# Kernel optimization log

Measured on AMD Instinct MI355X. Metric: run time of the kernel, lower is better.

Reference implementation:

```python
import jax, jax.numpy as jnp
import numpy as np

B, N, C, K = 8, 49104, 90, 1000  # batch, anchors, classes, pre-NMS top-k cap
NEG = -1e9


def _decode(reg, anc):
    # anchors ltrb -> cxcywh, apply reg, back to ltrb (matches decode_boxes)
    l, t, r, b = anc[..., 0], anc[..., 1], anc[..., 2], anc[..., 3]
    w_a, h_a = r - l, b - t
    cx_a, cy_a = l + w_a / 2, t + h_a / 2
    cx = cx_a + reg[..., 0] * w_a
    cy = cy_a + reg[..., 1] * h_a
    w = w_a * jnp.exp(reg[..., 2])
    h = h_a * jnp.exp(reg[..., 3])
    left, top = cx - w / 2, cy - h / 2
    return jnp.stack([left, top, left + w, top + h], -1)


def _iou(boxes):  # [K,4] -> [K,K]
    area = (boxes[:, 2] - boxes[:, 0]) * (boxes[:, 3] - boxes[:, 1])
    lt = jnp.maximum(boxes[:, None, :2], boxes[None, :, :2])
    rb = jnp.minimum(boxes[:, None, 2:], boxes[None, :, 2:])
    wh = jnp.clip(rb - lt, 0.0)
    inter = wh[..., 0] * wh[..., 1]
    return inter / (area[:, None] + area[None, :] - inter + 1e-9)


def _per_image(cls, reg, anchors, size, size_ori, score_thresh, nms_thresh):
    scores = jnp.max(cls, axis=-1)                       # [N]
    labels = jnp.argmax(cls, axis=-1).astype(jnp.int32)  # [N]
    valid = scores >= score_thresh
    boxes = _decode(reg, anchors)                        # [N,4] ltrb
    H = size[0].astype(jnp.float32)
    W = size[1].astype(jnp.float32)
    x = jnp.clip(boxes[..., 0::2], 0.0, W - 1.0)
    y = jnp.clip(boxes[..., 1::2], 0.0, H - 1.0)
    boxes = jnp.stack([x[..., 0], y[..., 0], x[..., 1], y[..., 1]], -1)
    # fixed-size substitute for nonzero(): take top-K by masked score
    ms = jnp.where(valid, scores, NEG)
    top_s, idx = jax.lax.top_k(ms, K)
    b, l, v = boxes[idx], labels[idx], valid[idx]        # [K,4],[K],[K]
    # batched_nms trick: offset boxes per class so classes never overlap
    off = l.astype(jnp.float32) * (jnp.maximum(W, H) + 1.0)
    iou = _iou(b + off[:, None])                         # [K,K]
    ar = jnp.arange(K)
    def body(i, supp):
        keep_i = v[i] & jnp.logical_not(supp[i])
        return supp | (keep_i & (iou[i] > nms_thresh) & (ar > i))
    supp = jax.lax.fori_loop(0, K, body, jnp.zeros((K,), bool))
    keep = v & jnp.logical_not(supp)
    scale = size_ori[0].astype(jnp.float32) / H
    b = b * scale
    out5 = jnp.concatenate(
        [jnp.where(keep[:, None], b, 0.0), jnp.where(keep, top_s, 0.0)[:, None]], -1)
    return out5, jnp.where(keep, l, -1), keep


def setup_inputs() -> dict:
    key = jax.random.key(0)
    k1, k2, k3, k4, k5, k6 = jax.random.split(key, 6)
    classifications = jax.random.uniform(k1, (B, N, C), dtype=jnp.float32)
    regressions = jax.random.normal(k2, (B, N, 4), dtype=jnp.float32) * 0.1
    cx = jax.random.uniform(k3, (N,), minval=0.0, maxval=512.0)
    cy = jax.random.uniform(k4, (N,), minval=0.0, maxval=512.0)
    w = jax.random.uniform(k5, (N,), minval=16.0, maxval=256.0)
    h = jax.random.uniform(k6, (N,), minval=16.0, maxval=256.0)
    anchors = jnp.stack([cx - w / 2, cy - h / 2, cx + w / 2, cy + h / 2], -1)
    return {
        'classifications': classifications,
        'regressions': regressions,
        'anchors': anchors,
        'image_sizes': jnp.full((B, 2), 512, dtype=jnp.int32),
        'image_sizes_ori': jnp.full((B, 2), 768, dtype=jnp.int32),
        'score_thresh': jnp.float32(0.999),
        'nms_thresh': jnp.float32(0.5),
    }


def reference(classifications, regressions, anchors, image_sizes, image_sizes_ori, score_thresh, nms_thresh):
    out5, labels, keep = jax.vmap(
        _per_image, in_axes=(0, 0, None, 0, 0, None, None))(
        classifications, regressions, anchors, image_sizes, image_sizes_ori,
        score_thresh, nms_thresh)
    return out5, labels, keep
```

## Files before the change

kernel.cpp:

```cpp
#include <hip/hip_runtime.h>
#include <stdint.h>

#define NB 8
#define NN 49104
#define NNP 49152
#define NC 90
#define NK 1000
#define KW 16
#define CAP2 8192
#define SEG 1024
#define CHUNK 6144
#define NB2 4352
#define NB2P 5120

typedef unsigned long long u64;

__global__ void k_score(const float* __restrict__ cls,
                        const float* __restrict__ thr_p,
                        u64* __restrict__ keys) {
  __shared__ float lds[64 * NC];
  int b = blockIdx.y;
  int t0 = blockIdx.x * 64;
  int acnt = NN - t0; if (acnt > 64) acnt = 64;
  const float4* src = (const float4*)(cls + ((size_t)b * NN + t0) * NC);
  float4* dst = (float4*)lds;
  int elems4 = acnt * NC / 4;
  for (int t = threadIdx.x; t < elems4; t += 256) dst[t] = src[t];
  __syncthreads();
  int a = threadIdx.x >> 2, q = threadIdx.x & 3;
  float best = -1e30f; int bc = 0;
  if (a < acnt) {
    for (int c = q; c < NC; c += 4) {
      float v = lds[a * NC + c];
      if (v > best) { best = v; bc = c; }
    }
    float ov; int oc;
    ov = __shfl_xor(best, 1); oc = __shfl_xor(bc, 1);
    if (ov > best || (ov == best && oc < bc)) { best = ov; bc = oc; }
    ov = __shfl_xor(best, 2); oc = __shfl_xor(bc, 2);
    if (ov > best || (ov == best && oc < bc)) { best = ov; bc = oc; }
  }
  if (q == 0) {
    unsigned idx = (unsigned)(t0 + a);
    u64 key = 0ULL;
    if (a < acnt && best >= *thr_p)
      key = ((u64)__float_as_uint(best) << 32) |
            ((u64)(0xFFFFu - idx) << 16) | (u64)(unsigned)bc;
    keys[(size_t)b * NNP + idx] = key;
  }
}

__global__ __launch_bounds__(1024) void k_compact(const u64* __restrict__ keys,
                                                  u64* __restrict__ ckeys) {
  __shared__ unsigned scnt;
  int tid = threadIdx.x;
  int lane = tid & 63;
  int b = blockIdx.y, chunk = blockIdx.x;
  if (tid == 0) scnt = 0u;
  __syncthreads();
  const u64* src = keys + (size_t)b * NNP + (size_t)chunk * CHUNK;
  u64* dst = ckeys + (size_t)b * CAP2 + (size_t)chunk * SEG;
  u64 k0 = src[tid], k1 = src[tid + 1024], k2 = src[tid + 2048];
  u64 k3 = src[tid + 3072], k4 = src[tid + 4096], k5 = src[tid + 5120];
  u64 lmask = (1ULL << lane) - 1ULL;
  u64 kk[6] = {k0, k1, k2, k3, k4, k5};
#pragma unroll
  for (int j = 0; j < 6; j++) {
    u64 key = kk[j];
    bool valid = key != 0ULL;
    u64 m = __ballot(valid);
    if (m) {
      int leader = (int)__ffsll((unsigned long long)m) - 1;
      unsigned base = 0;
      if (lane == leader) base = atomicAdd(&scnt, (unsigned)__popcll(m));
      base = __shfl(base, leader);
      if (valid) {
        unsigned pos = base + (unsigned)__popcll(m & lmask);
        if (pos < SEG) dst[pos] = key;
      }
    }
  }
  __syncthreads();
  unsigned total = scnt; if (total > SEG) total = SEG;
  for (unsigned t = total + tid; t < SEG; t += 1024) dst[t] = 0ULL;
}

__device__ __forceinline__ void decode_box(const float4 rg, const float4 an,
                                           float W, float H, float* out) {
#pragma clang fp contract(off)
  float l = an.x, t = an.y, r = an.z, bo = an.w;
  float wa = r - l, ha = bo - t;
  float cxa = l + wa * 0.5f, cya = t + ha * 0.5f;
  float cx = cxa + rg.x * wa;
  float cy = cya + rg.y * ha;
  float w = wa * expf(rg.z);
  float h = ha * expf(rg.w);
  float left = cx - w * 0.5f, top = cy - h * 0.5f;
  float right = left + w, botm = top + h;
  out[0] = fminf(fmaxf(left, 0.f), W - 1.f);
  out[1] = fminf(fmaxf(top, 0.f), H - 1.f);
  out[2] = fminf(fmaxf(right, 0.f), W - 1.f);
  out[3] = fminf(fmaxf(botm, 0.f), H - 1.f);
}

__global__ __launch_bounds__(1024) void k_sortsel(
    const u64* __restrict__ ckeys,
    const float* __restrict__ regs, const float* __restrict__ anch,
    const int* __restrict__ isz, const int* __restrict__ iszo,
    int* __restrict__ nvalid, float4* __restrict__ topoff,
    int* __restrict__ toplabel, float* __restrict__ out) {
  __shared__ u64 cand[CAP2];
  __shared__ u64 outk[CAP2];
  __shared__ unsigned hist[NB2P];
  __shared__ unsigned wsum[16];
  __shared__ unsigned scnt;
  int tid = threadIdx.x;
  int lane = tid & 63, wid = tid >> 6;
  int b = blockIdx.x;
  for (int i = tid; i < NB2P; i += 1024) hist[i] = 0u;
  if (tid == 0) scnt = 0u;
  __syncthreads();
  const ulonglong4* kv = (const ulonglong4*)(ckeys + (size_t)b * CAP2);
  ulonglong4 c0 = kv[tid], c1 = kv[tid + 1024];
  u64 lmask = (1ULL << lane) - 1ULL;
  u64 kk[8] = {c0.x, c0.y, c0.z, c0.w, c1.x, c1.y, c1.z, c1.w};
#pragma unroll
  for (int j = 0; j < 8; j++) {
    u64 key = kk[j];
    bool valid = key != 0ULL;
    u64 m = __ballot(valid);
    if (m) {
      int leader = (int)__ffsll((unsigned long long)m) - 1;
      unsigned base = 0;
      if (lane == leader) base = atomicAdd(&scnt, (unsigned)__popcll(m));
      base = __shfl(base, leader);
      if (valid) {
        unsigned pos = base + (unsigned)__popcll(m & lmask);
        if (pos < CAP2) cand[pos] = key;
        unsigned bin = (0x3F800000u - (unsigned)(key >> 32) - 1u) >> 2;
        if (bin >= NB2) bin = NB2 - 1;
        atomicAdd(&hist[bin], 1u);
      }
    }
  }
  __syncthreads();

  int base5 = tid * 5;
  unsigned mysum = 0;
#pragma unroll
  for (int i = 0; i < 5; i++) mysum += hist[base5 + i];
  unsigned v = mysum;
  for (int d = 1; d < 64; d <<= 1) {
    unsigned o = __shfl_up(v, d);
    if (lane >= d) v += o;
  }
  if (lane == 63) wsum[wid] = v;
  __syncthreads();
  if (tid == 0) {
    unsigned acc = 0;
    for (int w2 = 0; w2 < 16; w2++) { unsigned c = wsum[w2]; wsum[w2] = acc; acc += c; }
  }
  __syncthreads();
  unsigned running = wsum[wid] + v - mysum;
#pragma unroll
  for (int i = 0; i < 5; i++) {
    unsigned c = hist[base5 + i];
    hist[base5 + i] = running;
    running += c;
  }
  __syncthreads();

  unsigned total = scnt; if (total > CAP2) total = CAP2;
  for (unsigned p = tid; p < total; p += 1024) {
    u64 key = cand[p];
    unsigned bin = (0x3F800000u - (unsigned)(key >> 32) - 1u) >> 2;
    if (bin >= NB2) bin = NB2 - 1;
    unsigned pos = atomicAdd(&hist[bin], 1u);
    if (pos < CAP2) outk[pos] = key;
  }
  __syncthreads();

  for (int bin = tid; bin < NB2; bin += 1024) {
    unsigned hi = hist[bin];
    unsigned lo = bin ? hist[bin - 1] : 0u;
    if (hi > CAP2) hi = CAP2;
    if (lo > CAP2) lo = CAP2;
    if (hi > lo + 1) {
      for (unsigned i2 = lo + 1; i2 < hi; i2++) {
        u64 kx = outk[i2];
        int j = (int)i2 - 1;
        while (j >= (int)lo && outk[j] < kx) { outk[j + 1] = outk[j]; j--; }
        outk[j + 1] = kx;
      }
    }
  }
  __syncthreads();

  int n = (int)scnt; if (n > NK) n = NK;
  if (tid == 0) nvalid[b] = n;
  float H = (float)isz[b * 2 + 0];
  float W = (float)isz[b * 2 + 1];
  float scale = (float)iszo[b * 2 + 0] / H;
  float offmul = fmaxf(W, H) + 1.0f;
  for (int k = tid; k < n; k += 1024) {
    u64 key = outk[k];
    float sc = __uint_as_float((unsigned)(key >> 32));
    unsigned idx = 0xFFFFu - (unsigned)((key >> 16) & 0xFFFFull);
    int lab = (int)(key & 0xFFFFull);
    float raw[4];
    float4 rg = ((const float4*)regs)[(size_t)b * NN + idx];
    float4 an = ((const float4*)anch)[idx];
    decode_box(rg, an, W, H, raw);
    float off = (float)lab * offmul;
    topoff[(size_t)b * NK + k] =
        make_float4(raw[0] + off, raw[1] + off, raw[2] + off, raw[3] + off);
    toplabel[(size_t)b * NK + k] = lab;
    int g = b * NK + k;
    float* o5 = out + (size_t)g * 5;
    o5[0] = raw[0] * scale; o5[1] = raw[1] * scale;
    o5[2] = raw[2] * scale; o5[3] = raw[3] * scale;
    o5[4] = sc;
    out[(size_t)NB * NK * 5 + g] = (float)lab;
  }
}

__global__ __launch_bounds__(1024) void k_masknms(
    const float4* __restrict__ topoff, const int* __restrict__ toplabel,
    const int* __restrict__ nvalid, const float* __restrict__ thr_p,
    float* __restrict__ out) {
#pragma clang fp contract(off)
  __shared__ float4 bo[NK];
  __shared__ __align__(16) u64 sm[NK * KW];
  __shared__ unsigned short sidx[NK];
  __shared__ unsigned short send[NK];
  __shared__ int lcnt[NC + 1];
  __shared__ int lofs[NC + 1];
  __shared__ int lcur[NC];
  __shared__ u64 nzv[16];
  __shared__ u64 skeep[KW];
  int b = blockIdx.x;
  int tid = threadIdx.x;
  int n = nvalid[b];

  for (int t = tid; t < NK * KW; t += 1024) sm[t] = 0ULL;
  if (tid < 16) nzv[tid] = 0ULL;
  if (tid <= NC) lcnt[tid] = 0;
  for (int t = tid; t < NK; t += 1024) bo[t] = topoff[(size_t)b * NK + t];
  __syncthreads();

  for (int k = tid; k < n; k += 1024)
    atomicAdd(&lcnt[toplabel[(size_t)b * NK + k]], 1);
  __syncthreads();
  if (tid == 0) {
    int acc = 0;
    for (int c = 0; c < NC; c++) { lofs[c] = acc; acc += lcnt[c]; }
    lofs[NC] = acc;
  }
  __syncthreads();
  if (tid < NC) lcur[tid] = lofs[tid];
  __syncthreads();
  for (int k = tid; k < n; k += 1024) {
    int lab = toplabel[(size_t)b * NK + k];
    int pos = atomicAdd(&lcur[lab], 1);
    sidx[pos] = (unsigned short)k;
    send[pos] = (unsigned short)lofs[lab + 1];
  }
  __syncthreads();

  float thr = *thr_p;
  for (int p = tid; p < n; p += 1024) {
    int e = (int)send[p];
    int a = (int)sidx[p];
    for (int q = p + 1; q < e; q++) {
      int c2 = (int)sidx[q];
      int i = a < c2 ? a : c2;
      int j = a < c2 ? c2 : a;
      float4 B = bo[i];
      float4 C = bo[j];
      float x0 = B.x, y0 = B.y, x1 = B.z, y1 = B.w;
      float ai = (x1 - x0) * (y1 - y0);
      float aj = (C.z - C.x) * (C.w - C.y);
      float ltx = fmaxf(x0, C.x), lty = fmaxf(y0, C.y);
      float rbx = fminf(x1, C.z), rby = fminf(y1, C.w);
      float ww = fmaxf(rbx - ltx, 0.f), hh = fmaxf(rby - lty, 0.f);
      float inter = ww * hh;
      float den = ((ai + aj) - inter) + 1e-9f;
      float iou = inter / den;
      if (iou > thr) {
        atomicOr(&sm[(size_t)i * KW + (j >> 6)], 1ULL << (j & 63));
        atomicOr(&nzv[i >> 6], 1ULL << (i & 63));
      }
    }
  }
  __syncthreads();

  if (tid < 16) {
    int base = tid * 64;
    u64 validw;
    if (n <= base) validw = 0ULL;
    else if (n >= base + 64) validw = ~0ULL;
    else validw = (~0ULL) >> (64 - (n - base));
    nzv[tid] &= validw;
  }
  __syncthreads();

  int lane = tid & 63, ml = tid & 15;
  if (tid < 64) {
    int bb2 = ml * 64;
    u64 rem;
    if (n <= bb2) rem = ~0ULL;
    else if (n >= bb2 + 64) rem = 0ULL;
    else rem = (~0ULL) << (n - bb2);
    for (int w = 0; w < 16; w++) {
      unsigned rl = (unsigned)__builtin_amdgcn_readlane((int)(unsigned)rem, w);
      unsigned rh = (unsigned)__builtin_amdgcn_readlane((int)(unsigned)(rem >> 32), w);
      u64 rw = ((u64)rh << 32) | (u64)rl;
      u64 active = nzv[w] & ~rw;
      while (active) {
        int i = (int)__ffsll((unsigned long long)active) - 1;
        active &= active - 1ULL;
        u64 crow = sm[(size_t)(w * 64 + i) * KW + ml];
        rem |= crow;
        unsigned cl = (unsigned)__builtin_amdgcn_readlane((int)(unsigned)crow, w);
        unsigned ch = (unsigned)__builtin_amdgcn_readlane((int)(unsigned)(crow >> 32), w);
        rw |= ((u64)ch << 32) | (u64)cl;
        active &= ~rw;
      }
      if (lane == 0) skeep[w] = ~rw;
    }
  }
  __syncthreads();

  for (int k = tid; k < NK; k += 1024) {
    int g = b * NK + k;
    int keep = (int)((skeep[k >> 6] >> (k & 63)) & 1ULL);
    if (keep) {
      out[(size_t)NB * NK * 6 + g] = 1.0f;
    } else {
      float* o5 = out + (size_t)g * 5;
      o5[0] = 0.f; o5[1] = 0.f; o5[2] = 0.f; o5[3] = 0.f; o5[4] = 0.f;
      out[(size_t)NB * NK * 5 + g] = -1.0f;
      out[(size_t)NB * NK * 6 + g] = 0.0f;
    }
  }
}

extern "C" void kernel_launch(void* const* d_in, const int* in_sizes, int n_in,
                              void* d_out, int out_size, void* d_ws, size_t ws_size,
                              hipStream_t stream) {
  const float* cls = (const float*)d_in[0];
  const float* regs = (const float*)d_in[1];
  const float* anch = (const float*)d_in[2];
  const int* isz = (const int*)d_in[3];
  const int* iszo = (const int*)d_in[4];
  const float* sthr = (const float*)d_in[5];
  const float* nthr = (const float*)d_in[6];
  float* out = (float*)d_out;

  char* p = (char*)d_ws;
  auto alloc = [&](size_t bytes) {
    char* r = p;
    p += (bytes + 255) & ~(size_t)255;
    return r;
  };
  u64* keys = (u64*)alloc((size_t)NB * NNP * 8);
  u64* ckeys = (u64*)alloc((size_t)NB * CAP2 * 8);
  float4* topoff = (float4*)alloc((size_t)NB * NK * 16);
  int* toplabel = (int*)alloc((size_t)NB * NK * 4);
  int* nvalid = (int*)alloc((size_t)NB * 4);

  hipLaunchKernelGGL(k_score, dim3(NNP / 64, NB), dim3(256), 0, stream,
                     cls, sthr, keys);
  hipLaunchKernelGGL(k_compact, dim3(8, NB), dim3(1024), 0, stream,
                     keys, ckeys);
  hipLaunchKernelGGL(k_sortsel, dim3(NB), dim3(1024), 0, stream,
                     ckeys, regs, anch, isz, iszo, nvalid, topoff, toplabel, out);
  hipLaunchKernelGGL(k_masknms, dim3(NB), dim3(1024), 0, stream,
                     topoff, toplabel, nvalid, nthr, out);
}
```

Measured before the change: 59.64 us.

## Fuse compaction into scoring and merge sort-select with NMS kernel

```diff
diff --git a/kernel.cpp b/kernel.cpp
--- a/kernel.cpp
+++ b/kernel.cpp
@@ -9,7 +9,7 @@
 #define KW 16
 #define CAP2 8192
 #define SEG 1024
-#define CHUNK 6144
+#define BPC 96
 #define NB2 4352
 #define NB2P 5120
 
@@ -17,7 +17,8 @@
 
 __global__ void k_score(const float* __restrict__ cls,
                         const float* __restrict__ thr_p,
-                        u64* __restrict__ keys) {
+                        u64* __restrict__ ckeys,
+                        unsigned* __restrict__ segcnt) {
   __shared__ float lds[64 * NC];
   int b = blockIdx.y;
   int t0 = blockIdx.x * 64;
@@ -40,49 +41,28 @@
     ov = __shfl_xor(best, 2); oc = __shfl_xor(bc, 2);
     if (ov > best || (ov == best && oc < bc)) { best = ov; bc = oc; }
   }
-  if (q == 0) {
+  int lane = threadIdx.x & 63;
+  bool valid = (q == 0) && (a < acnt) && (best >= *thr_p);
+  u64 key = 0ULL;
+  if (valid) {
     unsigned idx = (unsigned)(t0 + a);
-    u64 key = 0ULL;
-    if (a < acnt && best >= *thr_p)
-      key = ((u64)__float_as_uint(best) << 32) |
-            ((u64)(0xFFFFu - idx) << 16) | (u64)(unsigned)bc;
-    keys[(size_t)b * NNP + idx] = key;
-  }
-}
-
-__global__ __launch_bounds__(1024) void k_compact(const u64* __restrict__ keys,
-                                                  u64* __restrict__ ckeys) {
-  __shared__ unsigned scnt;
-  int tid = threadIdx.x;
-  int lane = tid & 63;
-  int b = blockIdx.y, chunk = blockIdx.x;
-  if (tid == 0) scnt = 0u;
-  __syncthreads();
-  const u64* src = keys + (size_t)b * NNP + (size_t)chunk * CHUNK;
-  u64* dst = ckeys + (size_t)b * CAP2 + (size_t)chunk * SEG;
-  u64 k0 = src[tid], k1 = src[tid + 1024], k2 = src[tid + 2048];
-  u64 k3 = src[tid + 3072], k4 = src[tid + 4096], k5 = src[tid + 5120];
-  u64 lmask = (1ULL << lane) - 1ULL;
-  u64 kk[6] = {k0, k1, k2, k3, k4, k5};
-#pragma unroll
-  for (int j = 0; j < 6; j++) {
-    u64 key = kk[j];
-    bool valid = key != 0ULL;
-    u64 m = __ballot(valid);
-    if (m) {
-      int leader = (int)__ffsll((unsigned long long)m) - 1;
-      unsigned base = 0;
-      if (lane == leader) base = atomicAdd(&scnt, (unsigned)__popcll(m));
-      base = __shfl(base, leader);
-      if (valid) {
-        unsigned pos = base + (unsigned)__popcll(m & lmask);
-        if (pos < SEG) dst[pos] = key;
-      }
-    }
-  }
-  __syncthreads();
-  unsigned total = scnt; if (total > SEG) total = SEG;
-  for (unsigned t = total + tid; t < SEG; t += 1024) dst[t] = 0ULL;
+    key = ((u64)__float_as_uint(best) << 32) |
+          ((u64)(0xFFFFu - idx) << 16) | (u64)(unsigned)bc;
+  }
+  u64 m = __ballot(valid);
+  if (m) {
+    int leader = (int)__ffsll((unsigned long long)m) - 1;
+    int chunk = blockIdx.x / BPC;
+    unsigned base = 0;
+    if (lane == leader)
+      base = atomicAdd(&segcnt[b * 8 + chunk], (unsigned)__popcll(m));
+    base = __shfl(base, leader);
+    if (valid) {
+      unsigned pos = base + (unsigned)__popcll(m & ((1ULL << lane) - 1ULL));
+      if (pos < SEG)
+        ckeys[(size_t)b * CAP2 + (size_t)chunk * SEG + pos] = key;
+    }
+  }
 }
 
 __device__ __forceinline__ void decode_box(const float4 rg, const float4 an,
@@ -103,45 +83,52 @@
   out[3] = fminf(fmaxf(botm, 0.f), H - 1.f);
 }
 
-__global__ __launch_bounds__(1024) void k_sortsel(
-    const u64* __restrict__ ckeys,
+__global__ __launch_bounds__(1024) void k_sortnms(
+    const u64* __restrict__ ckeys, const unsigned* __restrict__ segcnt,
     const float* __restrict__ regs, const float* __restrict__ anch,
     const int* __restrict__ isz, const int* __restrict__ iszo,
-    int* __restrict__ nvalid, float4* __restrict__ topoff,
-    int* __restrict__ toplabel, float* __restrict__ out) {
-  __shared__ u64 cand[CAP2];
-  __shared__ u64 outk[CAP2];
-  __shared__ unsigned hist[NB2P];
+    const float* __restrict__ nthr_p, float* __restrict__ out) {
+#pragma clang fp contract(off)
+  __shared__ __align__(16) char S[151552];
   __shared__ unsigned wsum[16];
-  __shared__ unsigned scnt;
+  __shared__ unsigned sofs[9];
+  __shared__ int lcnt[NC + 1];
+  __shared__ int lofs[NC + 1];
+  __shared__ int lcur[NC];
+  __shared__ u64 nzv[16];
+  __shared__ u64 skeep[KW];
+
+  u64* cand = (u64*)S;
+  u64* outk = (u64*)(S + 65536);
+  unsigned* hist = (unsigned*)(S + 131072);
+
   int tid = threadIdx.x;
   int lane = tid & 63, wid = tid >> 6;
   int b = blockIdx.x;
+
   for (int i = tid; i < NB2P; i += 1024) hist[i] = 0u;
-  if (tid == 0) scnt = 0u;
-  __syncthreads();
-  const ulonglong4* kv = (const ulonglong4*)(ckeys + (size_t)b * CAP2);
-  ulonglong4 c0 = kv[tid], c1 = kv[tid + 1024];
-  u64 lmask = (1ULL << lane) - 1ULL;
-  u64 kk[8] = {c0.x, c0.y, c0.z, c0.w, c1.x, c1.y, c1.z, c1.w};
-#pragma unroll
-  for (int j = 0; j < 8; j++) {
-    u64 key = kk[j];
-    bool valid = key != 0ULL;
-    u64 m = __ballot(valid);
-    if (m) {
-      int leader = (int)__ffsll((unsigned long long)m) - 1;
-      unsigned base = 0;
-      if (lane == leader) base = atomicAdd(&scnt, (unsigned)__popcll(m));
-      base = __shfl(base, leader);
-      if (valid) {
-        unsigned pos = base + (unsigned)__popcll(m & lmask);
-        if (pos < CAP2) cand[pos] = key;
-        unsigned bin = (0x3F800000u - (unsigned)(key >> 32) - 1u) >> 2;
-        if (bin >= NB2) bin = NB2 - 1;
-        atomicAdd(&hist[bin], 1u);
-      }
-    }
+  if (tid == 0) {
+    unsigned acc = 0;
+    for (int s = 0; s < 8; s++) {
+      unsigned c = segcnt[b * 8 + s]; if (c > SEG) c = SEG;
+      sofs[s] = acc; acc += c;
+    }
+    sofs[8] = acc;
+  }
+  __syncthreads();
+  unsigned total = sofs[8];
+
+  for (int s = 0; s < 8; s++) {
+    unsigned o = sofs[s], c = sofs[s + 1] - o;
+    const u64* srcp = ckeys + (size_t)b * CAP2 + (size_t)s * SEG;
+    for (unsigned i = tid; i < c; i += 1024) cand[o + i] = srcp[i];
+  }
+  __syncthreads();
+
+  for (unsigned p = tid; p < total; p += 1024) {
+    unsigned bin = (0x3F800000u - (unsigned)(cand[p] >> 32) - 1u) >> 2;
+    if (bin >= NB2) bin = NB2 - 1;
+    atomicAdd(&hist[bin], 1u);
   }
   __syncthreads();
 
@@ -170,7 +157,6 @@
   }
   __syncthreads();
 
-  unsigned total = scnt; if (total > CAP2) total = CAP2;
   for (unsigned p = tid; p < total; p += 1024) {
     u64 key = cand[p];
     unsigned bin = (0x3F800000u - (unsigned)(key >> 32) - 1u) >> 2;
@@ -196,8 +182,13 @@
   }
   __syncthreads();
 
-  int n = (int)scnt; if (n > NK) n = NK;
-  if (tid == 0) nvalid[b] = n;
+  int n = (int)total; if (n > NK) n = NK;
+  float4* bo = (float4*)S;
+  unsigned short* llab = (unsigned short*)(S + 16000);
+  unsigned short* sidx = (unsigned short*)(S + 18000);
+  unsigned short* send = (unsigned short*)(S + 20000);
+  u64* sm = (u64*)(S + 22016);
+
   float H = (float)isz[b * 2 + 0];
   float W = (float)isz[b * 2 + 1];
   float scale = (float)iszo[b * 2 + 0] / H;
@@ -212,9 +203,8 @@
     float4 an = ((const float4*)anch)[idx];
     decode_box(rg, an, W, H, raw);
     float off = (float)lab * offmul;
-    topoff[(size_t)b * NK + k] =
-        make_float4(raw[0] + off, raw[1] + off, raw[2] + off, raw[3] + off);
-    toplabel[(size_t)b * NK + k] = lab;
+    bo[k] = make_float4(raw[0] + off, raw[1] + off, raw[2] + off, raw[3] + off);
+    llab[k] = (unsigned short)lab;
     int g = b * NK + k;
     float* o5 = out + (size_t)g * 5;
     o5[0] = raw[0] * scale; o5[1] = raw[1] * scale;
@@ -222,34 +212,14 @@
     o5[4] = sc;
     out[(size_t)NB * NK * 5 + g] = (float)lab;
   }
-}
-
-__global__ __launch_bounds__(1024) void k_masknms(
-    const float4* __restrict__ topoff, const int* __restrict__ toplabel,
-    const int* __restrict__ nvalid, const float* __restrict__ thr_p,
-    float* __restrict__ out) {
-#pragma clang fp contract(off)
-  __shared__ float4 bo[NK];
-  __shared__ __align__(16) u64 sm[NK * KW];
-  __shared__ unsigned short sidx[NK];
-  __shared__ unsigned short send[NK];
-  __shared__ int lcnt[NC + 1];
-  __shared__ int lofs[NC + 1];
-  __shared__ int lcur[NC];
-  __shared__ u64 nzv[16];
-  __shared__ u64 skeep[KW];
-  int b = blockIdx.x;
-  int tid = threadIdx.x;
-  int n = nvalid[b];
+  __syncthreads();
 
   for (int t = tid; t < NK * KW; t += 1024) sm[t] = 0ULL;
   if (tid < 16) nzv[tid] = 0ULL;
   if (tid <= NC) lcnt[tid] = 0;
-  for (int t = tid; t < NK; t += 1024) bo[t] = topoff[(size_t)b * NK + t];
-  __syncthreads();
-
-  for (int k = tid; k < n; k += 1024)
-    atomicAdd(&lcnt[toplabel[(size_t)b * NK + k]], 1);
+  __syncthreads();
+
+  for (int k = tid; k < n; k += 1024) atomicAdd(&lcnt[(int)llab[k]], 1);
   __syncthreads();
   if (tid == 0) {
     int acc = 0;
@@ -260,28 +230,28 @@
   if (tid < NC) lcur[tid] = lofs[tid];
   __syncthreads();
   for (int k = tid; k < n; k += 1024) {
-    int lab = toplabel[(size_t)b * NK + k];
+    int lab = (int)llab[k];
     int pos = atomicAdd(&lcur[lab], 1);
     sidx[pos] = (unsigned short)k;
     send[pos] = (unsigned short)lofs[lab + 1];
   }
   __syncthreads();
 
-  float thr = *thr_p;
+  float thr = *nthr_p;
   for (int p = tid; p < n; p += 1024) {
     int e = (int)send[p];
     int a = (int)sidx[p];
-    for (int q = p + 1; q < e; q++) {
-      int c2 = (int)sidx[q];
+    for (int q2 = p + 1; q2 < e; q2++) {
+      int c2 = (int)sidx[q2];
       int i = a < c2 ? a : c2;
       int j = a < c2 ? c2 : a;
-      float4 B = bo[i];
-      float4 C = bo[j];
-      float x0 = B.x, y0 = B.y, x1 = B.z, y1 = B.w;
+      float4 Bb = bo[i];
+      float4 Cc = bo[j];
+      float x0 = Bb.x, y0 = Bb.y, x1 = Bb.z, y1 = Bb.w;
       float ai = (x1 - x0) * (y1 - y0);
-      float aj = (C.z - C.x) * (C.w - C.y);
-      float ltx = fmaxf(x0, C.x), lty = fmaxf(y0, C.y);
-      float rbx = fminf(x1, C.z), rby = fminf(y1, C.w);
+      float aj = (Cc.z - Cc.x) * (Cc.w - Cc.y);
+      float ltx = fmaxf(x0, Cc.x), lty = fmaxf(y0, Cc.y);
+      float rbx = fminf(x1, Cc.z), rby = fminf(y1, Cc.w);
       float ww = fmaxf(rbx - ltx, 0.f), hh = fmaxf(rby - lty, 0.f);
       float inter = ww * hh;
       float den = ((ai + aj) - inter) + 1e-9f;
@@ -304,7 +274,7 @@
   }
   __syncthreads();
 
-  int lane = tid & 63, ml = tid & 15;
+  int ml = tid & 15;
   if (tid < 64) {
     int bb2 = ml * 64;
     u64 rem;
@@ -363,18 +333,12 @@
     p += (bytes + 255) & ~(size_t)255;
     return r;
   };
-  u64* keys = (u64*)alloc((size_t)NB * NNP * 8);
   u64* ckeys = (u64*)alloc((size_t)NB * CAP2 * 8);
-  float4* topoff = (float4*)alloc((size_t)NB * NK * 16);
-  int* toplabel = (int*)alloc((size_t)NB * NK * 4);
-  int* nvalid = (int*)alloc((size_t)NB * 4);
-
+  unsigned* segcnt = (unsigned*)alloc((size_t)NB * 8 * 4);
+
+  hipMemsetAsync(segcnt, 0, (size_t)NB * 8 * sizeof(unsigned), stream);
   hipLaunchKernelGGL(k_score, dim3(NNP / 64, NB), dim3(256), 0, stream,
-                     cls, sthr, keys);
-  hipLaunchKernelGGL(k_compact, dim3(8, NB), dim3(1024), 0, stream,
-                     keys, ckeys);
-  hipLaunchKernelGGL(k_sortsel, dim3(NB), dim3(1024), 0, stream,
-                     ckeys, regs, anch, isz, iszo, nvalid, topoff, toplabel, out);
-  hipLaunchKernelGGL(k_masknms, dim3(NB), dim3(1024), 0, stream,
-                     topoff, toplabel, nvalid, nthr, out);
+                     cls, sthr, ckeys, segcnt);
+  hipLaunchKernelGGL(k_sortnms, dim3(NB), dim3(1024), 0, stream,
+                     ckeys, segcnt, regs, anch, isz, iszo, nthr, out);
 }
```

Measured after the change: 217.2 us. +264.2%, slower.
